# Kernel optimization log

Measured on AMD Instinct MI355X. Metric: run time of the kernel, lower is better.

## Reference

```python
import jax, jax.numpy as jnp
import numpy as np

EPS = 1e-10


def setup_inputs() -> dict:
    key = jax.random.key(0)
    k1, k2, k3 = jax.random.split(key, 3)
    B, K, M, X, Y = 32, 4, 3, 256, 256
    predictions = jax.random.uniform(k1, (B, K, X, Y), dtype=jnp.float32)
    inputs = jax.random.normal(k2, (B, M, X, Y), dtype=jnp.float32)
    heart = jax.random.randint(k3, (B, 1, X, Y), 0, 2, dtype=jnp.int32)
    return {"predictions": predictions, "inputs": inputs, "heart": heart}


def reference(predictions, inputs, heart):
    # predictions: [B,K,X,Y] soft class maps; inputs: [B,M,X,Y]; heart: [B,1,X,Y] 0/1 ROI
    mask = (heart[:, 0] == 1).astype(predictions.dtype)            # [B,X,Y]
    n = jnp.sum(mask, axis=(-2, -1))                                # [B] masked pixel count
    pred = predictions * mask[:, None]                              # [B,K,X,Y] zero outside ROI
    # alpha[b,k] = mean of pred over masked pixels
    alpha = jnp.sum(pred, axis=(-2, -1)) / n[:, None]               # [B,K]
    s = jnp.sum(pred, axis=(-2, -1)) + EPS                          # [B,K]
    # weighted means mu[b,k,m] = sum(pred*inp)/ (sum(pred)+eps)
    mu = jnp.einsum('bkxy,bmxy->bkm', pred, inputs) / s[:, :, None]  # [B,K,M]
    diff = inputs[:, None] - mu[:, :, :, None, None]                 # [B,K,M,X,Y]
    var = jnp.einsum('bkmxy,bkxy->bkm', diff * diff, pred) / s[:, :, None] + EPS  # [B,K,M]
    # Gaussian pdf per (k,m), product over channels m (done in log-space, same math)
    v = var[:, :, :, None, None]
    log_pdf = -0.5 * jnp.log(2.0 * jnp.pi * v) - (diff * diff) / (2.0 * v)  # [B,K,M,X,Y]
    g = jnp.exp(jnp.sum(log_pdf, axis=2))                            # [B,K,X,Y] = prod_m pdf
    mix = jnp.sum(alpha[:, :, None, None] * g, axis=1)               # [B,X,Y]
    ll = jnp.log(mix + EPS)                                          # [B,X,Y]
    # mean of -log-likelihood over masked pixels per batch, then mean over batch
    per_b = -jnp.sum(mask * ll, axis=(-2, -1)) / n                   # [B]
    return jnp.mean(per_b)
```

## Files before the change

kernel.cpp:

```cpp
#include <hip/hip_runtime.h>

#define EPSF 1e-10f

constexpr int B = 32, K = 4, M = 3;
constexpr int NPIX = 256 * 256;
constexpr int BLOCKS_PER_B = 8;
constexpr int THREADS = 256;
constexpr int WAVES = THREADS / 64;
constexpr int CHUNKS = NPIX / (BLOCKS_PER_B * THREADS * 4);
constexpr int NVALS = 1 + K + 2 * K * M;

constexpr int OFF_N     = 0;
constexpr int OFF_W     = OFF_N + B;
constexpr int OFF_P     = OFF_W + B * K;
constexpr int OFF_Q     = OFF_P + B * K * M;
constexpr int OFF_ALPHA = OFF_Q + B * K * M;
constexpr int OFF_MU    = OFF_ALPHA + B * K;
constexpr int OFF_IV    = OFF_MU + B * K * M;
constexpr int OFF_CST   = OFF_IV + B * K * M;
constexpr int OFF_LL    = OFF_CST + B * K;
constexpr int WS_FLOATS = OFF_LL + B;

__device__ __forceinline__ float wave_reduce(float v) {
    #pragma unroll
    for (int off = 32; off > 0; off >>= 1) v += __shfl_down(v, off, 64);
    return v;
}

__global__ __launch_bounds__(THREADS) void pass1_kernel(
    const float* __restrict__ pred, const float* __restrict__ xin,
    const int* __restrict__ heart, float* __restrict__ ws) {
    const int b  = blockIdx.x / BLOCKS_PER_B;
    const int cb = blockIdx.x % BLOCKS_PER_B;

    float nacc = 0.0f;
    float Wk[K] = {};
    float Pa[K][M] = {};
    float Qa[K][M] = {};

    for (int it = 0; it < CHUNKS; ++it) {
        const int p0 = (((cb * CHUNKS + it) * THREADS) + threadIdx.x) * 4;

        const int4 h4 = *(const int4*)(heart + b * NPIX + p0);
        float mk[4];
        mk[0] = (h4.x == 1) ? 1.0f : 0.0f;
        mk[1] = (h4.y == 1) ? 1.0f : 0.0f;
        mk[2] = (h4.z == 1) ? 1.0f : 0.0f;
        mk[3] = (h4.w == 1) ? 1.0f : 0.0f;
        nacc += (mk[0] + mk[1]) + (mk[2] + mk[3]);

        float xv[M][4];
        #pragma unroll
        for (int m = 0; m < M; ++m) {
            float4 t = *(const float4*)(xin + (b * M + m) * NPIX + p0);
            xv[m][0] = t.x; xv[m][1] = t.y; xv[m][2] = t.z; xv[m][3] = t.w;
        }

        #pragma unroll
        for (int k = 0; k < K; ++k) {
            float4 pr = *(const float4*)(pred + (b * K + k) * NPIX + p0);
            float pm[4];
            pm[0] = pr.x * mk[0]; pm[1] = pr.y * mk[1];
            pm[2] = pr.z * mk[2]; pm[3] = pr.w * mk[3];
            Wk[k] += (pm[0] + pm[1]) + (pm[2] + pm[3]);
            #pragma unroll
            for (int m = 0; m < M; ++m) {
                #pragma unroll
                for (int j = 0; j < 4; ++j) {
                    float px = pm[j] * xv[m][j];
                    Pa[k][m] += px;
                    Qa[k][m] += px * xv[m][j];
                }
            }
        }
    }

    float vals[NVALS];
    vals[0] = nacc;
    #pragma unroll
    for (int k = 0; k < K; ++k) vals[1 + k] = Wk[k];
    #pragma unroll
    for (int k = 0; k < K; ++k)
        #pragma unroll
        for (int m = 0; m < M; ++m) {
            vals[1 + K + k * M + m]         = Pa[k][m];
            vals[1 + K + K * M + k * M + m] = Qa[k][m];
        }

    __shared__ float red[WAVES * NVALS];
    #pragma unroll
    for (int i = 0; i < NVALS; ++i) vals[i] = wave_reduce(vals[i]);
    const int wave = threadIdx.x >> 6;
    if ((threadIdx.x & 63) == 0) {
        #pragma unroll
        for (int i = 0; i < NVALS; ++i) red[wave * NVALS + i] = vals[i];
    }
    __syncthreads();
    const int i = threadIdx.x;
    if (i < NVALS) {
        float s = red[i];
        #pragma unroll
        for (int w = 1; w < WAVES; ++w) s += red[w * NVALS + i];
        int dst;
        if (i == 0)            dst = OFF_N + b;
        else if (i < 1 + K)    dst = OFF_W + b * K + (i - 1);
        else if (i < 1 + K + K * M) dst = OFF_P + b * K * M + (i - 1 - K);
        else                   dst = OFF_Q + b * K * M + (i - 1 - K - K * M);
        atomicAdd(&ws[dst], s);
    }
}

__global__ __launch_bounds__(128) void params_kernel(float* __restrict__ ws) {
    const int t = threadIdx.x;
    if (t >= B * K) return;
    const int b = t / K;
    const float n = ws[OFF_N + b];
    const float W = ws[OFF_W + t];
    const float s = W + EPSF;
    ws[OFF_ALPHA + t] = W / n;
    float cst = 0.0f;
    #pragma unroll
    for (int m = 0; m < M; ++m) {
        const float Pv = ws[OFF_P + t * M + m];
        const float Qv = ws[OFF_Q + t * M + m];
        const float mu = Pv / s;
        const float var = (Qv - 2.0f * mu * Pv + mu * mu * W) / s + EPSF;
        ws[OFF_MU + t * M + m] = mu;
        ws[OFF_IV + t * M + m] = 0.5f / var;
        cst -= 0.5f * logf(6.2831853071795864f * var);
    }
    ws[OFF_CST + t] = cst;
}

__global__ __launch_bounds__(THREADS) void pass2_kernel(
    const float* __restrict__ xin, const int* __restrict__ heart,
    float* __restrict__ ws) {
    const int b  = blockIdx.x / BLOCKS_PER_B;
    const int cb = blockIdx.x % BLOCKS_PER_B;

    float alpha[K], cst[K], mu[K][M], iv[K][M];
    #pragma unroll
    for (int k = 0; k < K; ++k) {
        alpha[k] = ws[OFF_ALPHA + b * K + k];
        cst[k]   = ws[OFF_CST + b * K + k];
        #pragma unroll
        for (int m = 0; m < M; ++m) {
            mu[k][m] = ws[OFF_MU + (b * K + k) * M + m];
            iv[k][m] = ws[OFF_IV + (b * K + k) * M + m];
        }
    }

    float acc = 0.0f;
    for (int it = 0; it < CHUNKS; ++it) {
        const int p0 = (((cb * CHUNKS + it) * THREADS) + threadIdx.x) * 4;

        const int4 h4 = *(const int4*)(heart + b * NPIX + p0);
        int hv[4] = {h4.x, h4.y, h4.z, h4.w};

        float xv[M][4];
        #pragma unroll
        for (int m = 0; m < M; ++m) {
            float4 t = *(const float4*)(xin + (b * M + m) * NPIX + p0);
            xv[m][0] = t.x; xv[m][1] = t.y; xv[m][2] = t.z; xv[m][3] = t.w;
        }

        #pragma unroll
        for (int j = 0; j < 4; ++j) {
            float mix = EPSF;
            #pragma unroll
            for (int k = 0; k < K; ++k) {
                float lp = cst[k];
                #pragma unroll
                for (int m = 0; m < M; ++m) {
                    float d = xv[m][j] - mu[k][m];
                    lp -= d * d * iv[k][m];
                }
                mix += alpha[k] * __expf(lp);
            }
            float mask = (hv[j] == 1) ? 1.0f : 0.0f;
            acc += mask * __logf(mix);
        }
    }

    __shared__ float red[WAVES];
    acc = wave_reduce(acc);
    const int wave = threadIdx.x >> 6;
    if ((threadIdx.x & 63) == 0) red[wave] = acc;
    __syncthreads();
    if (threadIdx.x == 0) {
        float s = red[0];
        #pragma unroll
        for (int w = 1; w < WAVES; ++w) s += red[w];
        atomicAdd(&ws[OFF_LL + b], s);
    }
}

__global__ void final_kernel(const float* __restrict__ ws, float* __restrict__ out) {
    if (threadIdx.x == 0 && blockIdx.x == 0) {
        float r = 0.0f;
        for (int b = 0; b < B; ++b) r += -ws[OFF_LL + b] / ws[OFF_N + b];
        out[0] = r / (float)B;
    }
}

extern "C" void kernel_launch(void* const* d_in, const int* in_sizes, int n_in,
                              void* d_out, int out_size, void* d_ws, size_t ws_size,
                              hipStream_t stream) {
    const float* pred  = (const float*)d_in[0];
    const float* xin   = (const float*)d_in[1];
    const int*   heart = (const int*)d_in[2];
    float* out = (float*)d_out;
    float* ws  = (float*)d_ws;

    hipMemsetAsync(d_ws, 0, WS_FLOATS * sizeof(float), stream);
    pass1_kernel<<<B * BLOCKS_PER_B, THREADS, 0, stream>>>(pred, xin, heart, ws);
    params_kernel<<<1, 128, 0, stream>>>(ws);
    pass2_kernel<<<B * BLOCKS_PER_B, THREADS, 0, stream>>>(xin, heart, ws);
    final_kernel<<<1, 64, 0, stream>>>(ws, out);
}
```

Before: 113.2 us.

## Raise grid parallelism and replace atomics with per-block partials

Grows the grid from 256 to 1024 blocks per pass (32 blocks per batch) so more of the GPU's compute units stay busy on this bandwidth-bound workload. Global atomicAdds are replaced by per-block partial sums written to workspace, which the params and final kernels then reduce. This also removes the memset launch. Chunk loops are fully unrolled. The trade-off is a slightly larger serial reduction in the single-block params kernel.

```diff
diff --git a/kernel.cpp b/kernel.cpp
--- a/kernel.cpp
+++ b/kernel.cpp
@@ -4,22 +4,19 @@
 
 constexpr int B = 32, K = 4, M = 3;
 constexpr int NPIX = 256 * 256;
-constexpr int BLOCKS_PER_B = 8;
+constexpr int BLOCKS_PER_B = 32;
 constexpr int THREADS = 256;
 constexpr int WAVES = THREADS / 64;
 constexpr int CHUNKS = NPIX / (BLOCKS_PER_B * THREADS * 4);
 constexpr int NVALS = 1 + K + 2 * K * M;
 
-constexpr int OFF_N     = 0;
-constexpr int OFF_W     = OFF_N + B;
-constexpr int OFF_P     = OFF_W + B * K;
-constexpr int OFF_Q     = OFF_P + B * K * M;
-constexpr int OFF_ALPHA = OFF_Q + B * K * M;
+constexpr int OFF_PART1 = 0;
+constexpr int OFF_PART2 = OFF_PART1 + B * BLOCKS_PER_B * NVALS;
+constexpr int OFF_ALPHA = OFF_PART2 + B * BLOCKS_PER_B;
 constexpr int OFF_MU    = OFF_ALPHA + B * K;
 constexpr int OFF_IV    = OFF_MU + B * K * M;
 constexpr int OFF_CST   = OFF_IV + B * K * M;
-constexpr int OFF_LL    = OFF_CST + B * K;
-constexpr int WS_FLOATS = OFF_LL + B;
+constexpr int OFF_NOUT  = OFF_CST + B * K;
 
 __device__ __forceinline__ float wave_reduce(float v) {
     #pragma unroll
@@ -38,6 +35,7 @@
     float Pa[K][M] = {};
     float Qa[K][M] = {};
 
+    #pragma unroll
     for (int it = 0; it < CHUNKS; ++it) {
         const int p0 = (((cb * CHUNKS + it) * THREADS) + threadIdx.x) * 4;
 
@@ -101,30 +99,35 @@
         float s = red[i];
         #pragma unroll
         for (int w = 1; w < WAVES; ++w) s += red[w * NVALS + i];
-        int dst;
-        if (i == 0)            dst = OFF_N + b;
-        else if (i < 1 + K)    dst = OFF_W + b * K + (i - 1);
-        else if (i < 1 + K + K * M) dst = OFF_P + b * K * M + (i - 1 - K);
-        else                   dst = OFF_Q + b * K * M + (i - 1 - K - K * M);
-        atomicAdd(&ws[dst], s);
-    }
-}
-
-__global__ __launch_bounds__(128) void params_kernel(float* __restrict__ ws) {
+        ws[OFF_PART1 + (b * BLOCKS_PER_B + cb) * NVALS + i] = s;
+    }
+}
+
+__global__ __launch_bounds__(B * K) void params_kernel(float* __restrict__ ws) {
     const int t = threadIdx.x;
-    if (t >= B * K) return;
     const int b = t / K;
-    const float n = ws[OFF_N + b];
-    const float W = ws[OFF_W + t];
+    const int k = t % K;
+
+    float n = 0.0f, W = 0.0f, P[M] = {}, Q[M] = {};
+    for (int p = 0; p < BLOCKS_PER_B; ++p) {
+        const float* base = ws + OFF_PART1 + (b * BLOCKS_PER_B + p) * NVALS;
+        n += base[0];
+        W += base[1 + k];
+        #pragma unroll
+        for (int m = 0; m < M; ++m) {
+            P[m] += base[1 + K + k * M + m];
+            Q[m] += base[1 + K + K * M + k * M + m];
+        }
+    }
+
     const float s = W + EPSF;
     ws[OFF_ALPHA + t] = W / n;
+    if (k == 0) ws[OFF_NOUT + b] = n;
     float cst = 0.0f;
     #pragma unroll
     for (int m = 0; m < M; ++m) {
-        const float Pv = ws[OFF_P + t * M + m];
-        const float Qv = ws[OFF_Q + t * M + m];
-        const float mu = Pv / s;
-        const float var = (Qv - 2.0f * mu * Pv + mu * mu * W) / s + EPSF;
+        const float mu = P[m] / s;
+        const float var = (Q[m] - 2.0f * mu * P[m] + mu * mu * W) / s + EPSF;
         ws[OFF_MU + t * M + m] = mu;
         ws[OFF_IV + t * M + m] = 0.5f / var;
         cst -= 0.5f * logf(6.2831853071795864f * var);
@@ -151,6 +154,7 @@
     }
 
     float acc = 0.0f;
+    #pragma unroll
     for (int it = 0; it < CHUNKS; ++it) {
         const int p0 = (((cb * CHUNKS + it) * THREADS) + threadIdx.x) * 4;
 
@@ -191,16 +195,22 @@
         float s = red[0];
         #pragma unroll
         for (int w = 1; w < WAVES; ++w) s += red[w];
-        atomicAdd(&ws[OFF_LL + b], s);
-    }
-}
-
-__global__ void final_kernel(const float* __restrict__ ws, float* __restrict__ out) {
-    if (threadIdx.x == 0 && blockIdx.x == 0) {
-        float r = 0.0f;
-        for (int b = 0; b < B; ++b) r += -ws[OFF_LL + b] / ws[OFF_N + b];
-        out[0] = r / (float)B;
-    }
+        ws[OFF_PART2 + b * BLOCKS_PER_B + cb] = s;
+    }
+}
+
+__global__ __launch_bounds__(64) void final_kernel(const float* __restrict__ ws,
+                                                   float* __restrict__ out) {
+    const int t = threadIdx.x;
+    float val = 0.0f;
+    if (t < B) {
+        float s = 0.0f;
+        for (int p = 0; p < BLOCKS_PER_B; ++p)
+            s += ws[OFF_PART2 + t * BLOCKS_PER_B + p];
+        val = -s / ws[OFF_NOUT + t];
+    }
+    val = wave_reduce(val);
+    if (t == 0) out[0] = val / (float)B;
 }
 
 extern "C" void kernel_launch(void* const* d_in, const int* in_sizes, int n_in,
@@ -212,9 +222,8 @@
     float* out = (float*)d_out;
     float* ws  = (float*)d_ws;
 
-    hipMemsetAsync(d_ws, 0, WS_FLOATS * sizeof(float), stream);
     pass1_kernel<<<B * BLOCKS_PER_B, THREADS, 0, stream>>>(pred, xin, heart, ws);
-    params_kernel<<<1, 128, 0, stream>>>(ws);
+    params_kernel<<<1, B * K, 0, stream>>>(ws);
     pass2_kernel<<<B * BLOCKS_PER_B, THREADS, 0, stream>>>(xin, heart, ws);
     final_kernel<<<1, 64, 0, stream>>>(ws, out);
 }
```

Result: no change. 113.3 us (+0.1%).
